# Performance work log

Measured on AMD Instinct MI355X. Metric: run time of the kernel, lower is better.

## Reference

```python
import jax, jax.numpy as jnp
import numpy as np

KR = 2  # nb_row == stride_row
KC = 2  # nb_col == stride_col


def setup_inputs() -> dict:
    key = jax.random.key(0)
    k1, k2, k3 = jax.random.split(key, 3)
    B, C, H, W_ = 32, 32, 128, 128
    F = 64
    OR, OC = H // KR, W_ // KC
    x = jax.random.normal(k1, (B, C, H, W_), dtype=jnp.float32)
    W = jax.random.normal(k2, (F, C, H, W_), dtype=jnp.float32) * 0.05
    b = jax.random.normal(k3, (OR, OC, F), dtype=jnp.float32) * 0.05
    return {"x": x, "W": W, "b": b}


def reference(x, W, b):
    # x: (B, C, H, W), W: (F, C, H, W) -- unshared per-pixel weights
    # per-pixel channel contraction: (B, F, H, W)
    out = jnp.einsum('bchw,fchw->bfhw', x, W)
    B, F, H, Wd = out.shape
    OR, OC = H // KR, Wd // KC
    # stride*avg_pool == exact sum over non-overlapping (KR, KC) patches
    out = out.reshape(B, F, OR, KR, OC, KC).sum(axis=(3, 5))
    # keras does a RAW reshape of b from (OR, OC, F) to (1, F, OR, OC)
    out = out + b.reshape(1, F, OR, OC)
    return jax.nn.relu(out)
```

## Files before the change

### kernel.cpp

```cpp
#include <hip/hip_runtime.h>
#include <stdint.h>


#define CC  32
#define HH  128
#define WWD 128
#define FF  64
#define ORR 64
#define OCC 64
#define CB  2
#define NIT (CC / CB)
#define CSTRIDE (CB * HH * WWD)

#define XBUF 4096
#define WBUF 8192

__global__ __launch_bounds__(1024, 4) void lc2d_kernel(
    const float* __restrict__ x, const float* __restrict__ wgt,
    const float* __restrict__ bias, float* __restrict__ out)
{
    __shared__ __align__(16) float Xs[2][XBUF];
    __shared__ __align__(16) float Ws[2][WBUF];

    const int tid = threadIdx.x;
    const int id  = blockIdx.x;
    const int oct = ((id & 1) << 1) | (id >> 7);
    const int orr = (id >> 1) & 63;
    const int w0  = oct * 32;
    const int h0  = orr * 2;

    const int lane = tid & 63;
    const int wv   = tid >> 6;
    const int chk  = lane & 7;
    const int sub  = lane >> 3;

    int r  = wv * 8 + sub;
    const float* gx  = x   + (((((r & 31) * CC) + (r >> 6)) * HH) + h0 + ((r >> 5) & 1)) * WWD + w0 + chk * 4;
    int r0 = wv * 8 + sub;
    const float* gw0 = wgt + (((((r0 & 63) * CC) + (r0 >> 7)) * HH) + h0 + ((r0 >> 6) & 1)) * WWD + w0 + chk * 4;
    int r1 = (wv + 16) * 8 + sub;
    const float* gw1 = wgt + (((((r1 & 63) * CC) + (r1 >> 7)) * HH) + h0 + ((r1 >> 6) & 1)) * WWD + w0 + chk * 4;

    auto issue = [&](int p) {
        __builtin_amdgcn_global_load_lds(
            (const __attribute__((address_space(1))) void*)gx,
            (__attribute__((address_space(3))) void*)(&Xs[p][wv * 256]), 16, 0, 0);
        __builtin_amdgcn_global_load_lds(
            (const __attribute__((address_space(1))) void*)gw0,
            (__attribute__((address_space(3))) void*)(&Ws[p][wv * 256]), 16, 0, 0);
        __builtin_amdgcn_global_load_lds(
            (const __attribute__((address_space(1))) void*)gw1,
            (__attribute__((address_space(3))) void*)(&Ws[p][4096 + wv * 256]), 16, 0, 0);
        gx += CSTRIDE; gw0 += CSTRIDE; gw1 += CSTRIDE;
    };

    issue(0);
    issue(1);

    const int ocg = tid & 7;
    const int bg  = (tid >> 3) & 7;
    const int fg  = wv;
    const int xoff = bg * 128 + ocg * 4;
    const int woff = fg * 128 + ocg * 4;

    float acc0[4][4], acc1[4][4];
#pragma unroll
    for (int i = 0; i < 4; ++i)
#pragma unroll
        for (int q = 0; q < 4; ++q) { acc0[i][q] = 0.f; acc1[i][q] = 0.f; }

    for (int it = 0; it < NIT; ++it) {
        const int p = it & 1;
        if (it == NIT - 1) __builtin_amdgcn_s_waitcnt(0x0F70);
        else               __builtin_amdgcn_s_waitcnt(0x0F73);
        __syncthreads();

        const float* Xp = Xs[p];
        const float* Wp = Ws[p];
#pragma unroll
        for (int s = 0; s < 2 * CB; ++s) {
            const float4* xr = (const float4*)(Xp + s * 1024 + xoff);
            const float4* wr = (const float4*)(Wp + s * 2048 + woff);
            float4 xa[4], wa[4];
#pragma unroll
            for (int i = 0; i < 4; ++i) xa[i] = xr[i * 8];
#pragma unroll
            for (int q = 0; q < 4; ++q) wa[q] = wr[q * 8];
#pragma unroll
            for (int i = 0; i < 4; ++i)
#pragma unroll
                for (int q = 0; q < 4; ++q) {
                    acc0[i][q] = fmaf(xa[i].x, wa[q].x, acc0[i][q]);
                    acc0[i][q] = fmaf(xa[i].y, wa[q].y, acc0[i][q]);
                    acc1[i][q] = fmaf(xa[i].z, wa[q].z, acc1[i][q]);
                    acc1[i][q] = fmaf(xa[i].w, wa[q].w, acc1[i][q]);
                }
        }
        __syncthreads();
        if (it + 2 < NIT) issue(p);
    }

    const int oc0 = oct * 16 + ocg * 2;
#pragma unroll
    for (int q = 0; q < 4; ++q) {
        const int f = fg * 4 + q;
        const float2 bv = *(const float2*)(bias + f * (ORR * OCC) + orr * OCC + oc0);
#pragma unroll
        for (int i = 0; i < 4; ++i) {
            const int b = bg * 4 + i;
            float2 o;
            o.x = fmaxf(acc0[i][q] + bv.x, 0.f);
            o.y = fmaxf(acc1[i][q] + bv.y, 0.f);
            *(float2*)(out + (((b * FF + f) * ORR + orr) * OCC) + oc0) = o;
        }
    }
}

extern "C" void kernel_launch(void* const* d_in, const int* in_sizes, int n_in,
                              void* d_out, int out_size, void* d_ws, size_t ws_size,
                              hipStream_t stream) {
    (void)in_sizes; (void)n_in; (void)d_ws; (void)ws_size; (void)out_size;
    const float* x    = (const float*)d_in[0];
    const float* wgt  = (const float*)d_in[1];
    const float* bias = (const float*)d_in[2];
    float* out        = (float*)d_out;
    lc2d_kernel<<<dim3(256, 1, 1), dim3(1024, 1, 1), 0, stream>>>(x, wgt, bias, out);
}
```

Baseline: 289.4 us.

## Load weights directly to registers, stage only x in LDS with larger channel block

Stops staging the per-pixel weights in LDS. Each thread now reads its four filter rows straight from global memory into registers, and only x tiles are staged in LDS, with the channel block doubled from 2 to 4. The LDS prefetch for the next block is issued at the top of each iteration, and x and weight register fragments are double-buffered across the inner loop, so there is one barrier per iteration instead of two. The aim is to cut LDS footprint and traffic and overlap loads with the FMAs. The cost is that the eight batch-group threads sharing a filter now read the same weight values from global memory separately, which depends on cache hits.

```diff
diff --git a/kernel.cpp b/kernel.cpp
--- a/kernel.cpp
+++ b/kernel.cpp
@@ -8,19 +8,17 @@
 #define FF  64
 #define ORR 64
 #define OCC 64
-#define CB  2
+#define CB  4
 #define NIT (CC / CB)
 #define CSTRIDE (CB * HH * WWD)
 
-#define XBUF 4096
-#define WBUF 8192
+#define XBUF 8192
 
 __global__ __launch_bounds__(1024, 4) void lc2d_kernel(
     const float* __restrict__ x, const float* __restrict__ wgt,
     const float* __restrict__ bias, float* __restrict__ out)
 {
     __shared__ __align__(16) float Xs[2][XBUF];
-    __shared__ __align__(16) float Ws[2][WBUF];
 
     const int tid = threadIdx.x;
     const int id  = blockIdx.x;
@@ -34,34 +32,30 @@
     const int chk  = lane & 7;
     const int sub  = lane >> 3;
 
-    int r  = wv * 8 + sub;
-    const float* gx  = x   + (((((r & 31) * CC) + (r >> 6)) * HH) + h0 + ((r >> 5) & 1)) * WWD + w0 + chk * 4;
-    int r0 = wv * 8 + sub;
-    const float* gw0 = wgt + (((((r0 & 63) * CC) + (r0 >> 7)) * HH) + h0 + ((r0 >> 6) & 1)) * WWD + w0 + chk * 4;
-    int r1 = (wv + 16) * 8 + sub;
-    const float* gw1 = wgt + (((((r1 & 63) * CC) + (r1 >> 7)) * HH) + h0 + ((r1 >> 6) & 1)) * WWD + w0 + chk * 4;
+    const int r0 = wv * 8 + sub;
+    const int r1 = 128 + wv * 8 + sub;
+    const float* gx0 = x + (((((r0 & 31) * CC) + (r0 >> 6)) * HH) + h0 + ((r0 >> 5) & 1)) * WWD + w0 + chk * 4;
+    const float* gx1 = x + (((((r1 & 31) * CC) + (r1 >> 6)) * HH) + h0 + ((r1 >> 5) & 1)) * WWD + w0 + chk * 4;
 
     auto issue = [&](int p) {
         __builtin_amdgcn_global_load_lds(
-            (const __attribute__((address_space(1))) void*)gx,
+            (const __attribute__((address_space(1))) void*)gx0,
             (__attribute__((address_space(3))) void*)(&Xs[p][wv * 256]), 16, 0, 0);
         __builtin_amdgcn_global_load_lds(
-            (const __attribute__((address_space(1))) void*)gw0,
-            (__attribute__((address_space(3))) void*)(&Ws[p][wv * 256]), 16, 0, 0);
-        __builtin_amdgcn_global_load_lds(
-            (const __attribute__((address_space(1))) void*)gw1,
-            (__attribute__((address_space(3))) void*)(&Ws[p][4096 + wv * 256]), 16, 0, 0);
-        gx += CSTRIDE; gw0 += CSTRIDE; gw1 += CSTRIDE;
+            (const __attribute__((address_space(1))) void*)gx1,
+            (__attribute__((address_space(3))) void*)(&Xs[p][4096 + wv * 256]), 16, 0, 0);
+        gx0 += CSTRIDE; gx1 += CSTRIDE;
     };
-
-    issue(0);
-    issue(1);
 
     const int ocg = tid & 7;
     const int bg  = (tid >> 3) & 7;
     const int fg  = wv;
     const int xoff = bg * 128 + ocg * 4;
-    const int woff = fg * 128 + ocg * 4;
+
+    const float* wq0 = wgt + ((fg * 4 + 0) * CC * HH + h0) * WWD + w0 + ocg * 4;
+    const float* wq1 = wq0 + CC * HH * WWD;
+    const float* wq2 = wq1 + CC * HH * WWD;
+    const float* wq3 = wq2 + CC * HH * WWD;
 
     float acc0[4][4], acc1[4][4];
 #pragma unroll
@@ -69,35 +63,50 @@
 #pragma unroll
         for (int q = 0; q < 4; ++q) { acc0[i][q] = 0.f; acc1[i][q] = 0.f; }
 
+    issue(0);
+    __syncthreads();
+
     for (int it = 0; it < NIT; ++it) {
         const int p = it & 1;
-        if (it == NIT - 1) __builtin_amdgcn_s_waitcnt(0x0F70);
-        else               __builtin_amdgcn_s_waitcnt(0x0F73);
-        __syncthreads();
+        if (it + 1 < NIT) issue(p ^ 1);
 
         const float* Xp = Xs[p];
-        const float* Wp = Ws[p];
+        float4 xa[2][4], wb[2][4];
+        {
+            const float4* xr = (const float4*)(Xp + xoff);
+#pragma unroll
+            for (int i = 0; i < 4; ++i) xa[0][i] = xr[i * 8];
+            wb[0][0] = *(const float4*)(wq0);
+            wb[0][1] = *(const float4*)(wq1);
+            wb[0][2] = *(const float4*)(wq2);
+            wb[0][3] = *(const float4*)(wq3);
+        }
 #pragma unroll
         for (int s = 0; s < 2 * CB; ++s) {
-            const float4* xr = (const float4*)(Xp + s * 1024 + xoff);
-            const float4* wr = (const float4*)(Wp + s * 2048 + woff);
-            float4 xa[4], wa[4];
+            const int cur = s & 1, nxt = cur ^ 1;
+            if (s + 1 < 2 * CB) {
+                const int sn  = s + 1;
+                const int off = ((sn >> 1) * HH + (sn & 1)) * WWD;
+                const float4* xr = (const float4*)(Xp + sn * 1024 + xoff);
 #pragma unroll
-            for (int i = 0; i < 4; ++i) xa[i] = xr[i * 8];
-#pragma unroll
-            for (int q = 0; q < 4; ++q) wa[q] = wr[q * 8];
+                for (int i = 0; i < 4; ++i) xa[nxt][i] = xr[i * 8];
+                wb[nxt][0] = *(const float4*)(wq0 + off);
+                wb[nxt][1] = *(const float4*)(wq1 + off);
+                wb[nxt][2] = *(const float4*)(wq2 + off);
+                wb[nxt][3] = *(const float4*)(wq3 + off);
+            }
 #pragma unroll
             for (int i = 0; i < 4; ++i)
 #pragma unroll
                 for (int q = 0; q < 4; ++q) {
-                    acc0[i][q] = fmaf(xa[i].x, wa[q].x, acc0[i][q]);
-                    acc0[i][q] = fmaf(xa[i].y, wa[q].y, acc0[i][q]);
-                    acc1[i][q] = fmaf(xa[i].z, wa[q].z, acc1[i][q]);
-                    acc1[i][q] = fmaf(xa[i].w, wa[q].w, acc1[i][q]);
+                    acc0[i][q] = fmaf(xa[cur][i].x, wb[cur][q].x, acc0[i][q]);
+                    acc0[i][q] = fmaf(xa[cur][i].y, wb[cur][q].y, acc0[i][q]);
+                    acc1[i][q] = fmaf(xa[cur][i].z, wb[cur][q].z, acc1[i][q]);
+                    acc1[i][q] = fmaf(xa[cur][i].w, wb[cur][q].w, acc1[i][q]);
                 }
         }
+        wq0 += CSTRIDE; wq1 += CSTRIDE; wq2 += CSTRIDE; wq3 += CSTRIDE;
         __syncthreads();
-        if (it + 2 < NIT) issue(p);
     }
 
     const int oc0 = oct * 16 + ocg * 2;
```

New measurement: 269.6 us. 6.8% less time.

## Split filters across two blocks and deepen the LDS pipeline to four stages

Applied to the files above, without the earlier changes.

The filter dimension is split in half across blocks, so the grid doubles to 512 blocks of 512 threads and each block handles 32 filters. The per-stage channel batch drops from two channels to one, and the prefetch ring grows from two to four stages, with explicit vmcnt waits and s_barrier calls fenced by sched_barrier. The aim is more blocks to fill the CUs and more loads in flight to hide global latency. In exchange, each x tile is now loaded by two blocks, which doubles x traffic, and each iteration does less work between barriers.

```diff
diff --git a/kernel.cpp b/kernel.cpp
--- a/kernel.cpp
+++ b/kernel.cpp
@@ -8,24 +8,23 @@
 #define FF  64
 #define ORR 64
 #define OCC 64
-#define CB  2
-#define NIT (CC / CB)
-#define CSTRIDE (CB * HH * WWD)
+#define NIT 32
+#define HW  (HH * WWD)
+#define CHW (CC * HH * WWD)
 
-#define XBUF 4096
-#define WBUF 8192
-
-__global__ __launch_bounds__(1024, 4) void lc2d_kernel(
+__global__ __launch_bounds__(512, 4) void lc2d_kernel(
     const float* __restrict__ x, const float* __restrict__ wgt,
     const float* __restrict__ bias, float* __restrict__ out)
 {
-    __shared__ __align__(16) float Xs[2][XBUF];
-    __shared__ __align__(16) float Ws[2][WBUF];
+    __shared__ __align__(16) float Xs[4][2048];
+    __shared__ __align__(16) float Ws[4][2048];
 
-    const int tid = threadIdx.x;
-    const int id  = blockIdx.x;
-    const int oct = ((id & 1) << 1) | (id >> 7);
-    const int orr = (id >> 1) & 63;
+    const int tid  = threadIdx.x;
+    const int id   = blockIdx.x;
+    const int fblk = id >> 8;
+    const int low  = id & 255;
+    const int oct = ((low & 1) << 1) | (low >> 7);
+    const int orr = (low >> 1) & 63;
     const int w0  = oct * 32;
     const int h0  = orr * 2;
 
@@ -34,34 +33,26 @@
     const int chk  = lane & 7;
     const int sub  = lane >> 3;
 
-    int r  = wv * 8 + sub;
-    const float* gx  = x   + (((((r & 31) * CC) + (r >> 6)) * HH) + h0 + ((r >> 5) & 1)) * WWD + w0 + chk * 4;
-    int r0 = wv * 8 + sub;
-    const float* gw0 = wgt + (((((r0 & 63) * CC) + (r0 >> 7)) * HH) + h0 + ((r0 >> 6) & 1)) * WWD + w0 + chk * 4;
-    int r1 = (wv + 16) * 8 + sub;
-    const float* gw1 = wgt + (((((r1 & 63) * CC) + (r1 >> 7)) * HH) + h0 + ((r1 >> 6) & 1)) * WWD + w0 + chk * 4;
+    const int r  = wv * 8 + sub;
+    const int sr = r >> 5;
+    const int br = r & 31;
+    const float* gx = x   + (((br * CC) * HH) + h0 + sr) * WWD + w0 + chk * 4;
+    const float* gw = wgt + ((((fblk * 32 + br) * CC) * HH) + h0 + sr) * WWD + w0 + chk * 4;
 
     auto issue = [&](int p) {
         __builtin_amdgcn_global_load_lds(
             (const __attribute__((address_space(1))) void*)gx,
             (__attribute__((address_space(3))) void*)(&Xs[p][wv * 256]), 16, 0, 0);
         __builtin_amdgcn_global_load_lds(
-            (const __attribute__((address_space(1))) void*)gw0,
+            (const __attribute__((address_space(1))) void*)gw,
             (__attribute__((address_space(3))) void*)(&Ws[p][wv * 256]), 16, 0, 0);
-        __builtin_amdgcn_global_load_lds(
-            (const __attribute__((address_space(1))) void*)gw1,
-            (__attribute__((address_space(3))) void*)(&Ws[p][4096 + wv * 256]), 16, 0, 0);
-        gx += CSTRIDE; gw0 += CSTRIDE; gw1 += CSTRIDE;
+        gx += HW; gw += HW;
     };
-
-    issue(0);
-    issue(1);
 
     const int ocg = tid & 7;
     const int bg  = (tid >> 3) & 7;
-    const int fg  = wv;
     const int xoff = bg * 128 + ocg * 4;
-    const int woff = fg * 128 + ocg * 4;
+    const int woff = wv * 128 + ocg * 4;
 
     float acc0[4][4], acc1[4][4];
 #pragma unroll
@@ -69,41 +60,50 @@
 #pragma unroll
         for (int q = 0; q < 4; ++q) { acc0[i][q] = 0.f; acc1[i][q] = 0.f; }
 
+    issue(0); issue(1); issue(2); issue(3);
+
     for (int it = 0; it < NIT; ++it) {
-        const int p = it & 1;
-        if (it == NIT - 1) __builtin_amdgcn_s_waitcnt(0x0F70);
-        else               __builtin_amdgcn_s_waitcnt(0x0F73);
-        __syncthreads();
+        const int rem = NIT - 1 - it;
+        if (rem >= 3)      asm volatile("s_waitcnt vmcnt(6)");
+        else if (rem == 2) asm volatile("s_waitcnt vmcnt(4)");
+        else if (rem == 1) asm volatile("s_waitcnt vmcnt(2)");
+        else               asm volatile("s_waitcnt vmcnt(0)");
+        __builtin_amdgcn_sched_barrier(0);
+        __builtin_amdgcn_s_barrier();
+        __builtin_amdgcn_sched_barrier(0);
 
+        const int p = it & 3;
         const float* Xp = Xs[p];
         const float* Wp = Ws[p];
 #pragma unroll
-        for (int s = 0; s < 2 * CB; ++s) {
+        for (int s = 0; s < 2; ++s) {
             const float4* xr = (const float4*)(Xp + s * 1024 + xoff);
-            const float4* wr = (const float4*)(Wp + s * 2048 + woff);
-            float4 xa[4], wa[4];
+            const float4* wr = (const float4*)(Wp + s * 1024 + woff);
+            float4 xa[4], wb[4];
 #pragma unroll
             for (int i = 0; i < 4; ++i) xa[i] = xr[i * 8];
 #pragma unroll
-            for (int q = 0; q < 4; ++q) wa[q] = wr[q * 8];
+            for (int q = 0; q < 4; ++q) wb[q] = wr[q * 8];
 #pragma unroll
             for (int i = 0; i < 4; ++i)
 #pragma unroll
                 for (int q = 0; q < 4; ++q) {
-                    acc0[i][q] = fmaf(xa[i].x, wa[q].x, acc0[i][q]);
-                    acc0[i][q] = fmaf(xa[i].y, wa[q].y, acc0[i][q]);
-                    acc1[i][q] = fmaf(xa[i].z, wa[q].z, acc1[i][q]);
-                    acc1[i][q] = fmaf(xa[i].w, wa[q].w, acc1[i][q]);
+                    acc0[i][q] = fmaf(xa[i].x, wb[q].x, acc0[i][q]);
+                    acc0[i][q] = fmaf(xa[i].y, wb[q].y, acc0[i][q]);
+                    acc1[i][q] = fmaf(xa[i].z, wb[q].z, acc1[i][q]);
+                    acc1[i][q] = fmaf(xa[i].w, wb[q].w, acc1[i][q]);
                 }
         }
-        __syncthreads();
-        if (it + 2 < NIT) issue(p);
+        __builtin_amdgcn_sched_barrier(0);
+        __builtin_amdgcn_s_barrier();
+        __builtin_amdgcn_sched_barrier(0);
+        if (it + 4 < NIT) issue(p);
     }
 
     const int oc0 = oct * 16 + ocg * 2;
 #pragma unroll
     for (int q = 0; q < 4; ++q) {
-        const int f = fg * 4 + q;
+        const int f = fblk * 32 + wv * 4 + q;
         const float2 bv = *(const float2*)(bias + f * (ORR * OCC) + orr * OCC + oc0);
 #pragma unroll
         for (int i = 0; i < 4; ++i) {
@@ -124,5 +124,5 @@
     const float* wgt  = (const float*)d_in[1];
     const float* bias = (const float*)d_in[2];
     float* out        = (float*)d_out;
-    lc2d_kernel<<<dim3(256, 1, 1), dim3(1024, 1, 1), 0, stream>>>(x, wgt, bias, out);
+    lc2d_kernel<<<dim3(512, 1, 1), dim3(512, 1, 1), 0, stream>>>(x, wgt, bias, out);
 }
```

New measurement: 263.4 us. 1.1x faster.
